# Optimization experiments

Measured on AMD Instinct MI355X. Metric: run time of the kernel, lower is better.

Reference implementation:

```python
import jax, jax.numpy as jnp
import numpy as np

D_MODEL = 1024
N_HEADS = 16
HEAD_DIM = D_MODEL // N_HEADS
B, S = 4, 2048


def setup_inputs() -> dict:
    key = jax.random.key(0)
    ks = jax.random.split(key, 12)
    s = 1.0 / np.sqrt(D_MODEL)
    inp = {
        'query': jax.random.normal(ks[0], (B, S, D_MODEL), jnp.float32),
        'key': jax.random.normal(ks[1], (B, S, D_MODEL), jnp.float32),
        'value': jax.random.normal(ks[2], (B, S, D_MODEL), jnp.float32),
        # causal mask, broadcast over batch and heads: [1,1,S,S]
        'mask': jnp.tril(jnp.ones((S, S), jnp.int32))[None, None],
        'Wq': jax.random.normal(ks[3], (D_MODEL, D_MODEL), jnp.float32) * s,
        'bq': jnp.zeros((D_MODEL,), jnp.float32),
        'Wk': jax.random.normal(ks[4], (D_MODEL, D_MODEL), jnp.float32) * s,
        'bk': jnp.zeros((D_MODEL,), jnp.float32),
        'Wv': jax.random.normal(ks[5], (D_MODEL, D_MODEL), jnp.float32) * s,
        'bv': jnp.zeros((D_MODEL,), jnp.float32),
        'Wo': jax.random.normal(ks[6], (D_MODEL, D_MODEL), jnp.float32) * s,
        'bo': jnp.zeros((D_MODEL,), jnp.float32),
    }
    return inp


def reference(query, key, value, mask, Wq, bq, Wk, bk, Wv, bv, Wo, bo):
    b, q_len, _ = query.shape
    scale = jnp.sqrt(jnp.float32(HEAD_DIM))
    # projections
    q = query @ Wq + bq
    k = key @ Wk + bk
    v = value @ Wv + bv
    # [b, h, s, hd]
    q = q.reshape(b, q_len, N_HEADS, HEAD_DIM).transpose(0, 2, 1, 3)
    k = k.reshape(b, -1, N_HEADS, HEAD_DIM).transpose(0, 2, 1, 3)
    v = v.reshape(b, -1, N_HEADS, HEAD_DIM).transpose(0, 2, 1, 3)
    scores = jnp.einsum('bhqd,bhkd->bhqk', q, k) / scale
    scores = jnp.where(mask == 0, jnp.float32(-jnp.inf), scores)
    attn = jax.nn.softmax(scores, axis=-1)  # dropout p=0 / eval mode
    out = jnp.einsum('bhqk,bhkd->bhqd', attn, v)
    out = out.transpose(0, 2, 1, 3).reshape(b, q_len, D_MODEL)
    return out @ Wo + bo
```

## Files before the change

kernel.cpp:

```cpp
#include <hip/hip_runtime.h>
#include <hip/hip_bf16.h>

typedef __attribute__((ext_vector_type(8))) short short8;
typedef __attribute__((ext_vector_type(4))) float floatx4;
typedef __attribute__((ext_vector_type(4))) unsigned short ushort4v;

#define D_MODEL 1024
#define S_LEN   2048
#define N_HEADS 16
#define HEAD_DIM 64
#define BATCH   4

__device__ __forceinline__ unsigned short f2bf(float x) {
    union { float f; unsigned int u; } v; v.f = x;
    unsigned int u = v.u;
    unsigned int r = (u + 0x7FFFu + ((u >> 16) & 1u)) >> 16;
    return (unsigned short)r;
}
__device__ __forceinline__ unsigned short f2bf_trunc(float x) {
    union { float f; unsigned int u; } v; v.f = x;
    return (unsigned short)(v.u >> 16);
}

__device__ __forceinline__ void gload_lds16(const void* g, void* s) {
    __builtin_amdgcn_global_load_lds(
        (const __attribute__((address_space(1))) void*)g,
        (__attribute__((address_space(3))) void*)s, 16, 0, 0);
}

struct Conv3 {
    const float* src[3];
    unsigned short* dst[3];
};

__global__ __launch_bounds__(256) void conv_bf16(Conv3 a) {
    const float* s = a.src[blockIdx.z];
    unsigned short* d = a.dst[blockIdx.z];
    size_t i = ((size_t)blockIdx.x * 256 + threadIdx.x) * 8;
    float4 f0 = *(const float4*)(s + i);
    float4 f1 = *(const float4*)(s + i + 4);
    short8 v;
    v[0] = (short)f2bf(f0.x); v[1] = (short)f2bf(f0.y);
    v[2] = (short)f2bf(f0.z); v[3] = (short)f2bf(f0.w);
    v[4] = (short)f2bf(f1.x); v[5] = (short)f2bf(f1.y);
    v[6] = (short)f2bf(f1.z); v[7] = (short)f2bf(f1.w);
    *(short8*)(d + i) = v;
}

struct Trans4 {
    const float* W[4];
    unsigned short* Wt[4];
};

__global__ __launch_bounds__(256) void transpose_w(Trans4 args) {
    __shared__ unsigned short tile[32][33];
    const float* W = args.W[blockIdx.z];
    unsigned short* Wt = args.Wt[blockIdx.z];
    int n0 = blockIdx.x * 32;
    int k0 = blockIdx.y * 32;
    int t = threadIdx.x;
    int r = t >> 5, c = t & 31;
    for (int i = 0; i < 4; ++i) {
        int k = k0 + r + i * 8;
        tile[r + i * 8][c] = f2bf(W[(size_t)k * D_MODEL + n0 + c]);
    }
    __syncthreads();
    for (int i = 0; i < 4; ++i) {
        int n = n0 + r + i * 8;
        Wt[(size_t)n * D_MODEL + k0 + c] = tile[c][r + i * 8];
    }
}

struct GemmIn {
    const unsigned short* A;
    const unsigned short* Bt;
    const float* bias;
    void* C;
    int mode;
    float scale;
};
struct Gemm3 { GemmIn g[3]; };

#define BAR()   asm volatile("s_barrier" ::: "memory")
#define LGKM0() asm volatile("s_waitcnt lgkmcnt(0)" ::: "memory")
#define VMW2()  asm volatile("s_waitcnt vmcnt(2)" ::: "memory")
#define VMW0()  asm volatile("s_waitcnt vmcnt(0)" ::: "memory")

#define READ_A4(BUF)                                                           \
    _Pragma("unroll") for (int ii = 0; ii < 4; ++ii) {                         \
        aF[ii][0] = *(const short8*)&lds[(BUF)*16384 + aOff + ii*512];         \
        aF[ii][1] = *(const short8*)&lds[(BUF)*16384 + aOff + ii*512 + 4096];  \
    }
#define READ_B4(BUF)                                                           \
    _Pragma("unroll") for (int jj = 0; jj < 4; ++jj) {                         \
        bF[jj][0] = *(const short8*)&lds[(BUF)*16384 + bOff + jj*512];         \
        bF[jj][1] = *(const short8*)&lds[(BUF)*16384 + bOff + jj*512 + 4096];  \
    }
#define MFMA_ALL()                                                             \
    __builtin_amdgcn_s_setprio(1);                                             \
    _Pragma("unroll") for (int ii = 0; ii < 4; ++ii)                           \
    _Pragma("unroll") for (int jj = 0; jj < 4; ++jj) {                         \
        acc[ii][jj] = __builtin_amdgcn_mfma_f32_16x16x32_bf16(                 \
            aF[ii][0], bF[jj][0], acc[ii][jj], 0, 0, 0);                       \
        acc[ii][jj] = __builtin_amdgcn_mfma_f32_16x16x32_bf16(                 \
            aF[ii][1], bF[jj][1], acc[ii][jj], 0, 0, 0);                       \
    }                                                                          \
    __builtin_amdgcn_s_setprio(0)

__global__ __launch_bounds__(256, 2) void gemm_128(Gemm3 args) {
    constexpr int K = D_MODEL, N = D_MODEL;
    constexpr int NT = K / 64;
    GemmIn g = args.g[blockIdx.z];

    __shared__ __align__(16) unsigned short lds[32768];

    const int m0 = blockIdx.x * 128;
    const int n0 = blockIdx.y * 128;
    const int t = threadIdx.x;
    const int w = t >> 6, lane = t & 63;
    const int quad = lane >> 4, l16 = lane & 15;
    const int wm = w >> 1, wn = w & 1;

    const int srow = w * 32 + (lane >> 2);
    const int scol = ((lane & 3) * 8) ^ ((lane & 32) ? 16 : 0);

    const int fx = (quad * 8) ^ ((l16 & 8) ? 16 : 0);
    const int aOff = (wm * 64 + l16) * 32 + fx;
    const int bOff = 8192 + (wn * 64 + l16) * 32 + fx;

    floatx4 acc[4][4] = {};
    short8 aF[4][2], bF[4][2];

    auto stageA = [&](int buf, int kt) {
        const unsigned short* s0 = g.A + (size_t)(m0 + srow) * K + kt * 64 + scol;
        unsigned short* d0 = &lds[buf * 16384 + (w * 32) * 32];
        gload_lds16(s0, d0);
        gload_lds16(s0 + 32, d0 + 4096);
        gload_lds16(s0 + (size_t)16 * K, d0 + 512);
        gload_lds16(s0 + (size_t)16 * K + 32, d0 + 512 + 4096);
    };
    auto stageB = [&](int buf, int kt) {
        const unsigned short* s0 = g.Bt + (size_t)(n0 + srow) * K + kt * 64 + scol;
        unsigned short* d0 = &lds[buf * 16384 + 8192 + (w * 32) * 32];
        gload_lds16(s0, d0);
        gload_lds16(s0 + 32, d0 + 4096);
        gload_lds16(s0 + (size_t)16 * K, d0 + 512);
        gload_lds16(s0 + (size_t)16 * K + 32, d0 + 512 + 4096);
    };

    stageA(0, 0); stageB(0, 0);
    VMW0();
    BAR();

#pragma unroll 2
    for (int kt = 0; kt < NT; ++kt) {
        const int buf = kt & 1;
        if (kt + 1 < NT) { stageA(buf ^ 1, kt + 1); stageB(buf ^ 1, kt + 1); }
        READ_A4(buf); READ_B4(buf);
        LGKM0();
        MFMA_ALL();
        if (kt + 1 < NT) { VMW0(); BAR(); }
    }

    if (g.mode == 2) {
        unsigned short* Ct = (unsigned short*)g.C;
#pragma unroll
        for (int j = 0; j < 4; ++j) {
            int col = n0 + wn * 64 + j * 16 + l16;
            int h = col >> 6, dd = col & 63;
            float bv = g.bias[col];
#pragma unroll
            for (int i = 0; i < 4; ++i) {
                int row0 = m0 + wm * 64 + i * 16 + quad * 4;
                int bb = row0 >> 11, s = row0 & 2047;
                ushort4v u;
#pragma unroll
                for (int r = 0; r < 4; ++r) u[r] = f2bf((acc[i][j][r] + bv) * g.scale);
                *(ushort4v*)(Ct + ((size_t)(bb * 16 + h) * 64 + dd) * 2048 + s) = u;
            }
        }
    } else {
#pragma unroll
        for (int j = 0; j < 4; ++j) {
            int col = n0 + wn * 64 + j * 16 + l16;
            float bv = g.bias[col];
#pragma unroll
            for (int i = 0; i < 4; ++i) {
#pragma unroll
                for (int r = 0; r < 4; ++r) {
                    int row = m0 + wm * 64 + i * 16 + quad * 4 + r;
                    float v = (acc[i][j][r] + bv) * g.scale;
                    if (g.mode == 1)
                        ((float*)g.C)[(size_t)row * N + col] = v;
                    else
                        ((unsigned short*)g.C)[(size_t)row * N + col] = f2bf(v);
                }
            }
        }
    }
}

__global__ __launch_bounds__(512) void flash_attn(
    const unsigned short* __restrict__ Qp,
    const unsigned short* __restrict__ Kp,
    const unsigned short* __restrict__ Vtg,
    unsigned short* __restrict__ Op) {
    constexpr int S = S_LEN, D = D_MODEL;
    __shared__ __align__(16) unsigned short Ks[2 * 4096];
    __shared__ __align__(16) unsigned short Vs[2 * 4096];
    __shared__ __align__(16) unsigned short Ps[8][1024];

    int id = blockIdx.x + (blockIdx.y << 3);
    int pair = (id >> 3) & 7;
    int bh = (id & 7) | ((id >> 6) << 3);
    int b = bh >> 4;
    int t = threadIdx.x;
    int wave = t >> 6, lane = t & 63;
    int quad = lane >> 4, l16 = lane & 15;

    const size_t head_off = (size_t)b * S * D + (size_t)(bh & 15) * HEAD_DIM;
    const unsigned short* Khead = Kp + head_off;
    const unsigned short* Vhead = Vtg + (size_t)bh * 64 * S;

    int q0l = pair * 128, q0h = (15 - pair) * 128;
    int qgl = q0l + wave * 16 + l16;
    int qgh = q0h + wave * 16 + l16;

    const unsigned short* qpl = Qp + head_off + (size_t)qgl * D + quad * 8;
    short8 ql0 = *(const short8*)qpl, ql1 = *(const short8*)(qpl + 32);
    const unsigned short* qph = Qp + head_off + (size_t)qgh * D + quad * 8;
    short8 qh0 = *(const short8*)qph, qh1 = *(const short8*)(qph + 32);

    floatx4 ol[4] = {}, oh[4] = {};
    floatx4 lsl = {}, lsh = {};

    short8 a1;
#pragma unroll
    for (int e = 0; e < 8; ++e) a1[e] = (l16 == 0) ? (short)0x3F80 : (short)0;

    int sw = wave & 3;
    bool doK = wave < 4;
    int srow = sw * 16 + (lane >> 2);
    int scol = ((lane & 3) * 8) ^ ((lane & 32) ? 16 : 0);

    auto stage = [&](int buf, int k0) {
        if (doK) {
            const unsigned short* s0 = Khead + (size_t)(k0 + srow) * D + scol;
            unsigned short* d0 = Ks + buf * 4096 + sw * 512;
            gload_lds16(s0, d0);
            gload_lds16(s0 + 32, d0 + 2048);
        } else {
            const unsigned short* s0 = Vhead + (size_t)srow * S + k0 + scol;
            unsigned short* d0 = Vs + buf * 4096 + sw * 512;
            gload_lds16(s0, d0);
            gload_lds16(s0 + 32, d0 + 2048);
        }
    };

    int wqminl = q0l + wave * 16, wqmaxl = wqminl + 15;
    int wqminh = q0h + wave * 16, wqmaxh = wqminh + 15;

    const int swz = (quad * 8) ^ ((l16 & 8) ? 16 : 0);
    const int pr = ((l16 & 8) ? 16 : 0) ^ ((l16 & 6) << 2);
    unsigned short* pw = &Ps[wave][0];

    auto half_step = [&](const unsigned short* Kb, const unsigned short* Vb,
                         int k0, int qg, int wqmin, floatx4& ls,
                         floatx4* o, short8 qb0, short8 qb1) {
        floatx4 st[4];
        __builtin_amdgcn_s_setprio(1);
        for (int gk = 0; gk < 4; ++gk) {
            short8 ka0 = *(const short8*)&Kb[(gk * 16 + l16) * 32 + swz];
            short8 ka1 = *(const short8*)&Kb[2048 + (gk * 16 + l16) * 32 + swz];
            floatx4 s = {};
            s = __builtin_amdgcn_mfma_f32_16x16x32_bf16(ka0, qb0, s, 0, 0, 0);
            s = __builtin_amdgcn_mfma_f32_16x16x32_bf16(ka1, qb1, s, 0, 0, 0);
            st[gk] = s;
        }
        __builtin_amdgcn_s_setprio(0);

        float sv[16];
        if (k0 + 63 < wqmin) {
            for (int i = 0; i < 16; ++i)
                sv[i] = __builtin_amdgcn_exp2f(st[i >> 2][i & 3]);
        } else {
            for (int gk = 0; gk < 4; ++gk)
                for (int r = 0; r < 4; ++r) {
                    int key = k0 + gk * 16 + quad * 4 + r;
                    sv[gk * 4 + r] = (key <= qg)
                        ? __builtin_amdgcn_exp2f(st[gk][r]) : 0.f;
                }
        }

        for (int gk = 0; gk < 4; ++gk) {
            ushort4v u;
            for (int r = 0; r < 4; ++r) u[r] = f2bf_trunc(sv[gk * 4 + r]);
            *(ushort4v*)&pw[(gk >> 1) * 512 + l16 * 32 +
                            ((((gk & 1) * 16) + quad * 4) ^ pr)] = u;
        }

        short8 pf0 = *(const short8*)&pw[l16 * 32 + ((quad * 8) ^ pr)];
        short8 pf1 = *(const short8*)&pw[512 + l16 * 32 + ((quad * 8) ^ pr)];
        __builtin_amdgcn_s_setprio(1);
        ls = __builtin_amdgcn_mfma_f32_16x16x32_bf16(a1, pf0, ls, 0, 0, 0);
        ls = __builtin_amdgcn_mfma_f32_16x16x32_bf16(a1, pf1, ls, 0, 0, 0);
        for (int jd = 0; jd < 4; ++jd) {
            short8 va0 = *(const short8*)&Vb[(jd * 16 + l16) * 32 + swz];
            short8 va1 = *(const short8*)&Vb[2048 + (jd * 16 + l16) * 32 + swz];
            o[jd] = __builtin_amdgcn_mfma_f32_16x16x32_bf16(va0, pf0, o[jd], 0, 0, 0);
            o[jd] = __builtin_amdgcn_mfma_f32_16x16x32_bf16(va1, pf1, o[jd], 0, 0, 0);
        }
        __builtin_amdgcn_s_setprio(0);
    };

    int n_kt = 2 * (15 - pair) + 2;
    stage(0, 0);
    for (int kt = 0; kt < n_kt; ++kt) {
        int k0 = kt * 64;
        if (kt + 1 < n_kt) {
            stage((kt + 1) & 1, k0 + 64);
            VMW2();
        } else {
            VMW0();
        }
        BAR();

        const unsigned short* Kb = Ks + (kt & 1) * 4096;
        const unsigned short* Vb = Vs + (kt & 1) * 4096;
        if (k0 <= wqmaxl) half_step(Kb, Vb, k0, qgl, wqminl, lsl, ol, ql0, ql1);
        if (k0 <= wqmaxh) half_step(Kb, Vb, k0, qgh, wqminh, lsh, oh, qh0, qh1);
        BAR();
    }

    {
        float inv = 1.0f / __shfl(lsl[0], l16);
        unsigned short* op = Op + head_off + (size_t)qgl * D;
        for (int jd = 0; jd < 4; ++jd) {
            ushort4v u;
            for (int r = 0; r < 4; ++r) u[r] = f2bf(ol[jd][r] * inv);
            *(ushort4v*)(op + jd * 16 + quad * 4) = u;
        }
    }
    {
        float inv = 1.0f / __shfl(lsh[0], l16);
        unsigned short* op = Op + head_off + (size_t)qgh * D;
        for (int jd = 0; jd < 4; ++jd) {
            ushort4v u;
            for (int r = 0; r < 4; ++r) u[r] = f2bf(oh[jd][r] * inv);
            *(ushort4v*)(op + jd * 16 + quad * 4) = u;
        }
    }
}

extern "C" void kernel_launch(void* const* d_in, const int* in_sizes, int n_in,
                              void* d_out, int out_size, void* d_ws,
                              size_t ws_size, hipStream_t stream) {
    const float* query = (const float*)d_in[0];
    const float* key   = (const float*)d_in[1];
    const float* value = (const float*)d_in[2];
    const float* Wq = (const float*)d_in[4];
    const float* bq = (const float*)d_in[5];
    const float* Wk = (const float*)d_in[6];
    const float* bk = (const float*)d_in[7];
    const float* Wv = (const float*)d_in[8];
    const float* bv = (const float*)d_in[9];
    const float* Wo = (const float*)d_in[10];
    const float* bo = (const float*)d_in[11];
    float* out = (float*)d_out;

    char* ws = (char*)d_ws;
    const size_t WT_SZ = (size_t)D_MODEL * D_MODEL * 2;
    const size_t X_SZ = (size_t)BATCH * S_LEN * D_MODEL * 2;
    unsigned short* wtq = (unsigned short*)(ws);
    unsigned short* wtk = (unsigned short*)(ws + WT_SZ);
    unsigned short* wtv = (unsigned short*)(ws + 2 * WT_SZ);
    unsigned short* wto = (unsigned short*)(ws + 3 * WT_SZ);
    unsigned short* Qbf = (unsigned short*)(ws + 4 * WT_SZ);
    unsigned short* Kbf = (unsigned short*)(ws + 4 * WT_SZ + X_SZ);
    unsigned short* Vbf = (unsigned short*)(ws + 4 * WT_SZ + 2 * X_SZ);
    unsigned short* Qp  = (unsigned short*)(ws + 4 * WT_SZ + 3 * X_SZ);
    unsigned short* Kp  = (unsigned short*)(ws + 4 * WT_SZ + 4 * X_SZ);
    unsigned short* Vtg = (unsigned short*)(ws + 4 * WT_SZ + 5 * X_SZ);
    unsigned short* Ao  = Qbf;

    Trans4 ta;
    ta.W[0] = Wq; ta.W[1] = Wk; ta.W[2] = Wv; ta.W[3] = Wo;
    ta.Wt[0] = wtq; ta.Wt[1] = wtk; ta.Wt[2] = wtv; ta.Wt[3] = wto;
    transpose_w<<<dim3(32, 32, 4), 256, 0, stream>>>(ta);

    Conv3 ca;
    ca.src[0] = query; ca.src[1] = key; ca.src[2] = value;
    ca.dst[0] = Qbf;   ca.dst[1] = Kbf; ca.dst[2] = Vbf;
    conv_bf16<<<dim3(4096, 1, 3), 256, 0, stream>>>(ca);

    const float q_scale = 0.125f * 1.44269504088896340736f;
    Gemm3 gq;
    gq.g[0].A = Qbf; gq.g[0].Bt = wtq; gq.g[0].bias = bq; gq.g[0].C = Qp;  gq.g[0].mode = 0; gq.g[0].scale = q_scale;
    gq.g[1].A = Kbf; gq.g[1].Bt = wtk; gq.g[1].bias = bk; gq.g[1].C = Kp;  gq.g[1].mode = 0; gq.g[1].scale = 1.0f;
    gq.g[2].A = Vbf; gq.g[2].Bt = wtv; gq.g[2].bias = bv; gq.g[2].C = Vtg; gq.g[2].mode = 2; gq.g[2].scale = 1.0f;
    gemm_128<<<dim3(64, 8, 3), 256, 0, stream>>>(gq);

    flash_attn<<<dim3(8, BATCH * N_HEADS), 512, 0, stream>>>(
        Qp, Kp, Vtg, Ao);

    Gemm3 go;
    go.g[0].A = Ao; go.g[0].Bt = wto; go.g[0].bias = bo; go.g[0].C = out; go.g[0].mode = 1; go.g[0].scale = 1.0f;
    gemm_128<<<dim3(64, 8, 1), 256, 0, stream>>>(go);
}
```

Baseline: 318.4 us.

## Fuse fp32-to-bf16 input conversion into QKV projection GEMM A-tile loading

Drops the standalone conversion kernel and has the projection GEMM load fp32 activations through registers, convert them with packed bf16 instructions, and store them to LDS. This removes a full read/write pass over the three input tensors and one launch. In exchange, the GEMM reads twice the A bytes per tile and replaces async global-to-LDS loads with a register path that waits on loads before writing LDS, which may expose latency.

```diff
diff --git a/kernel.cpp b/kernel.cpp
--- a/kernel.cpp
+++ b/kernel.cpp
@@ -4,6 +4,7 @@
 typedef __attribute__((ext_vector_type(8))) short short8;
 typedef __attribute__((ext_vector_type(4))) float floatx4;
 typedef __attribute__((ext_vector_type(4))) unsigned short ushort4v;
+typedef __attribute__((ext_vector_type(4))) unsigned int uint4v;
 
 #define D_MODEL 1024
 #define S_LEN   2048
@@ -21,30 +22,16 @@
     union { float f; unsigned int u; } v; v.f = x;
     return (unsigned short)(v.u >> 16);
 }
+__device__ __forceinline__ unsigned int cvt_pk_bf16(float lo, float hi) {
+    unsigned int r;
+    asm volatile("v_cvt_pk_bf16_f32 %0, %1, %2" : "=v"(r) : "v"(lo), "v"(hi));
+    return r;
+}
 
 __device__ __forceinline__ void gload_lds16(const void* g, void* s) {
     __builtin_amdgcn_global_load_lds(
         (const __attribute__((address_space(1))) void*)g,
         (__attribute__((address_space(3))) void*)s, 16, 0, 0);
-}
-
-struct Conv3 {
-    const float* src[3];
-    unsigned short* dst[3];
-};
-
-__global__ __launch_bounds__(256) void conv_bf16(Conv3 a) {
-    const float* s = a.src[blockIdx.z];
-    unsigned short* d = a.dst[blockIdx.z];
-    size_t i = ((size_t)blockIdx.x * 256 + threadIdx.x) * 8;
-    float4 f0 = *(const float4*)(s + i);
-    float4 f1 = *(const float4*)(s + i + 4);
-    short8 v;
-    v[0] = (short)f2bf(f0.x); v[1] = (short)f2bf(f0.y);
-    v[2] = (short)f2bf(f0.z); v[3] = (short)f2bf(f0.w);
-    v[4] = (short)f2bf(f1.x); v[5] = (short)f2bf(f1.y);
-    v[6] = (short)f2bf(f1.z); v[7] = (short)f2bf(f1.w);
-    *(short8*)(d + i) = v;
 }
 
 struct Trans4 {
@@ -72,11 +59,12 @@
 }
 
 struct GemmIn {
-    const unsigned short* A;
+    const void* A;
     const unsigned short* Bt;
     const float* bias;
     void* C;
     int mode;
+    int a_fp32;
     float scale;
 };
 struct Gemm3 { GemmIn g[3]; };
@@ -101,11 +89,12 @@
     _Pragma("unroll") for (int ii = 0; ii < 4; ++ii)                           \
     _Pragma("unroll") for (int jj = 0; jj < 4; ++jj) {                         \
         acc[ii][jj] = __builtin_amdgcn_mfma_f32_16x16x32_bf16(                 \
-            aF[ii][0], bF[jj][0], acc[ii][jj], 0, 0, 0);                       \
+            acc_a[ii][0], bF[jj][0], acc[ii][jj], 0, 0, 0);                    \
         acc[ii][jj] = __builtin_amdgcn_mfma_f32_16x16x32_bf16(                 \
-            aF[ii][1], bF[jj][1], acc[ii][jj], 0, 0, 0);                       \
+            acc_a[ii][1], bF[jj][1], acc[ii][jj], 0, 0, 0);                    \
     }                                                                          \
     __builtin_amdgcn_s_setprio(0)
+#define acc_a aF
 
 __global__ __launch_bounds__(256, 2) void gemm_128(Gemm3 args) {
     constexpr int K = D_MODEL, N = D_MODEL;
@@ -131,8 +120,12 @@
     floatx4 acc[4][4] = {};
     short8 aF[4][2], bF[4][2];
 
+    const unsigned short* A16 = (const unsigned short*)g.A;
+    const float* A32 = (const float*)g.A;
+    const bool afp = g.a_fp32 != 0;
+
     auto stageA = [&](int buf, int kt) {
-        const unsigned short* s0 = g.A + (size_t)(m0 + srow) * K + kt * 64 + scol;
+        const unsigned short* s0 = A16 + (size_t)(m0 + srow) * K + kt * 64 + scol;
         unsigned short* d0 = &lds[buf * 16384 + (w * 32) * 32];
         gload_lds16(s0, d0);
         gload_lds16(s0 + 32, d0 + 4096);
@@ -148,18 +141,62 @@
         gload_lds16(s0 + (size_t)16 * K + 32, d0 + 512 + 4096);
     };
 
-    stageA(0, 0); stageB(0, 0);
-    VMW0();
+    float4 aLd[8];
+    auto loadA32 = [&](int kt) {
+#pragma unroll
+        for (int rg = 0; rg < 2; ++rg)
+#pragma unroll
+            for (int c = 0; c < 2; ++c) {
+                const float* s0 = A32 +
+                    (size_t)(m0 + w * 32 + rg * 16 + (lane >> 2)) * K +
+                    kt * 64 + c * 32 + (lane & 3) * 8;
+                aLd[(rg * 2 + c) * 2]     = *(const float4*)s0;
+                aLd[(rg * 2 + c) * 2 + 1] = *(const float4*)(s0 + 4);
+            }
+    };
+    auto writeA32 = [&](int buf) {
+#pragma unroll
+        for (int rg = 0; rg < 2; ++rg)
+#pragma unroll
+            for (int c = 0; c < 2; ++c) {
+                float4 f0 = aLd[(rg * 2 + c) * 2];
+                float4 f1 = aLd[(rg * 2 + c) * 2 + 1];
+                uint4v v;
+                v.x = cvt_pk_bf16(f0.x, f0.y);
+                v.y = cvt_pk_bf16(f0.z, f0.w);
+                v.z = cvt_pk_bf16(f1.x, f1.y);
+                v.w = cvt_pk_bf16(f1.z, f1.w);
+                *(uint4v*)&lds[buf * 16384 + c * 4096 +
+                               (w * 32 + rg * 16 + (lane >> 2)) * 32 + scol] = v;
+            }
+    };
+
+    if (afp) {
+        loadA32(0); stageB(0, 0);
+        VMW0();
+        writeA32(0);
+        LGKM0();
+    } else {
+        stageA(0, 0); stageB(0, 0);
+        VMW0();
+    }
     BAR();
 
 #pragma unroll 2
     for (int kt = 0; kt < NT; ++kt) {
         const int buf = kt & 1;
-        if (kt + 1 < NT) { stageA(buf ^ 1, kt + 1); stageB(buf ^ 1, kt + 1); }
+        if (kt + 1 < NT) {
+            if (afp) loadA32(kt + 1); else stageA(buf ^ 1, kt + 1);
+            stageB(buf ^ 1, kt + 1);
+        }
         READ_A4(buf); READ_B4(buf);
         LGKM0();
         MFMA_ALL();
-        if (kt + 1 < NT) { VMW0(); BAR(); }
+        if (kt + 1 < NT) {
+            VMW0();
+            if (afp) { writeA32(buf ^ 1); LGKM0(); }
+            BAR();
+        }
     }
 
     if (g.mode == 2) {
@@ -375,35 +412,27 @@
     unsigned short* wtk = (unsigned short*)(ws + WT_SZ);
     unsigned short* wtv = (unsigned short*)(ws + 2 * WT_SZ);
     unsigned short* wto = (unsigned short*)(ws + 3 * WT_SZ);
-    unsigned short* Qbf = (unsigned short*)(ws + 4 * WT_SZ);
-    unsigned short* Kbf = (unsigned short*)(ws + 4 * WT_SZ + X_SZ);
-    unsigned short* Vbf = (unsigned short*)(ws + 4 * WT_SZ + 2 * X_SZ);
-    unsigned short* Qp  = (unsigned short*)(ws + 4 * WT_SZ + 3 * X_SZ);
-    unsigned short* Kp  = (unsigned short*)(ws + 4 * WT_SZ + 4 * X_SZ);
-    unsigned short* Vtg = (unsigned short*)(ws + 4 * WT_SZ + 5 * X_SZ);
-    unsigned short* Ao  = Qbf;
+    unsigned short* Qp  = (unsigned short*)(ws + 4 * WT_SZ);
+    unsigned short* Kp  = (unsigned short*)(ws + 4 * WT_SZ + X_SZ);
+    unsigned short* Vtg = (unsigned short*)(ws + 4 * WT_SZ + 2 * X_SZ);
+    unsigned short* Ao  = (unsigned short*)(ws + 4 * WT_SZ + 3 * X_SZ);
 
     Trans4 ta;
     ta.W[0] = Wq; ta.W[1] = Wk; ta.W[2] = Wv; ta.W[3] = Wo;
     ta.Wt[0] = wtq; ta.Wt[1] = wtk; ta.Wt[2] = wtv; ta.Wt[3] = wto;
     transpose_w<<<dim3(32, 32, 4), 256, 0, stream>>>(ta);
 
-    Conv3 ca;
-    ca.src[0] = query; ca.src[1] = key; ca.src[2] = value;
-    ca.dst[0] = Qbf;   ca.dst[1] = Kbf; ca.dst[2] = Vbf;
-    conv_bf16<<<dim3(4096, 1, 3), 256, 0, stream>>>(ca);
-
     const float q_scale = 0.125f * 1.44269504088896340736f;
     Gemm3 gq;
-    gq.g[0].A = Qbf; gq.g[0].Bt = wtq; gq.g[0].bias = bq; gq.g[0].C = Qp;  gq.g[0].mode = 0; gq.g[0].scale = q_scale;
-    gq.g[1].A = Kbf; gq.g[1].Bt = wtk; gq.g[1].bias = bk; gq.g[1].C = Kp;  gq.g[1].mode = 0; gq.g[1].scale = 1.0f;
-    gq.g[2].A = Vbf; gq.g[2].Bt = wtv; gq.g[2].bias = bv; gq.g[2].C = Vtg; gq.g[2].mode = 2; gq.g[2].scale = 1.0f;
+    gq.g[0].A = query; gq.g[0].Bt = wtq; gq.g[0].bias = bq; gq.g[0].C = Qp;  gq.g[0].mode = 0; gq.g[0].a_fp32 = 1; gq.g[0].scale = q_scale;
+    gq.g[1].A = key;   gq.g[1].Bt = wtk; gq.g[1].bias = bk; gq.g[1].C = Kp;  gq.g[1].mode = 0; gq.g[1].a_fp32 = 1; gq.g[1].scale = 1.0f;
+    gq.g[2].A = value; gq.g[2].Bt = wtv; gq.g[2].bias = bv; gq.g[2].C = Vtg; gq.g[2].mode = 2; gq.g[2].a_fp32 = 1; gq.g[2].scale = 1.0f;
     gemm_128<<<dim3(64, 8, 3), 256, 0, stream>>>(gq);
 
     flash_attn<<<dim3(8, BATCH * N_HEADS), 512, 0, stream>>>(
         Qp, Kp, Vtg, Ao);
 
     Gemm3 go;
-    go.g[0].A = Ao; go.g[0].Bt = wto; go.g[0].bias = bo; go.g[0].C = out; go.g[0].mode = 1; go.g[0].scale = 1.0f;
+    go.g[0].A = Ao; go.g[0].Bt = wto; go.g[0].bias = bo; go.g[0].C = out; go.g[0].mode = 1; go.g[0].a_fp32 = 0; go.g[0].scale = 1.0f;
     gemm_128<<<dim3(64, 8, 1), 256, 0, stream>>>(go);
 }
```

After: 320.9 us. No clear change (+0.8%).
